# Optimization experiments

Hardware: AMD Instinct MI355X
Metric: run time of the kernel (lower is better)

Reference implementation:

```python
import jax, jax.numpy as jnp
import numpy as np

C = 1.0                      # Poincare ball curvature (pmath.project k=1.0)
SQRT_C = jnp.float32(np.sqrt(C))
MIN_NORM = 1e-15
BALL_EPS = 4e-3              # geoopt float32 boundary eps


def _norm(x):
    return jnp.clip(jnp.linalg.norm(x, axis=-1, keepdims=True), MIN_NORM, None)


def _artanh(x):
    return jnp.arctanh(jnp.clip(x, -1 + 1e-7, 1 - 1e-7))


def logmap0(x):
    # tangent vector at origin: artanh(sqrt(c)||x||) * x / (sqrt(c)||x||)
    n = _norm(x)
    return _artanh(SQRT_C * n) * x / (SQRT_C * n)


def expmap0(u):
    # point on ball: tanh(sqrt(c)||u||) * u / (sqrt(c)||u||)
    n = _norm(u)
    return jnp.tanh(SQRT_C * n) * u / (SQRT_C * n)


def project(x):
    # clip to open ball of radius (1-eps)/sqrt(c)
    n = _norm(x)
    maxnorm = (1.0 - BALL_EPS) / SQRT_C
    return jnp.where(n > maxnorm, x * (maxnorm / n), x)


def setup_inputs() -> dict:
    key = jax.random.key(0)
    k1, k2 = jax.random.split(key)
    B, N, D = 2, 8192, 256
    # valid Poincare-ball points: small tangent vectors mapped onto the ball
    x = project(expmap0(0.1 * jax.random.normal(k1, (B, N, D), dtype=jnp.float32)))
    # row-normalized-ish dense adjacency standing in for the sparse adj
    adj = jax.random.uniform(k2, (B, N, N), dtype=jnp.float32) / N
    return {"x": x, "adj": adj}


def reference(x, adj) -> jnp.ndarray:
    # HypAgg.forward: aggregate in tangent space at origin, map back, project
    x_tangent = logmap0(x)                          # [B, N, D]
    support_t = jnp.einsum("bij,bjd->bid", adj, x_tangent)  # batched spmm
    return project(expmap0(support_t))              # [B, N, D]
```

## Files before the change

kernel.cpp:

```cpp
#include <hip/hip_runtime.h>

#define BATCH 2
#define NN 8192
#define DD 256
#define BK 64

typedef __attribute__((ext_vector_type(8))) short bf16x8;
typedef __attribute__((ext_vector_type(4))) float f32x4;

__device__ __forceinline__ unsigned short f2bf(float f) {
    unsigned u = __builtin_bit_cast(unsigned, f);
    u += 0x7fffu + ((u >> 16) & 1u);
    return (unsigned short)(u >> 16);
}

__global__ void k_logmap_scale(const float* __restrict__ x, float* __restrict__ scale) {
    int row = blockIdx.x;
    int lane = threadIdx.x;
    const float4* xr = (const float4*)(x + (size_t)row * DD);
    float4 v = xr[lane];
    float s = v.x * v.x + v.y * v.y + v.z * v.z + v.w * v.w;
#pragma unroll
    for (int m = 1; m < 64; m <<= 1) s += __shfl_xor(s, m, 64);
    if (lane == 0) {
        float n = sqrtf(s);
        n = fmaxf(n, 1e-15f);
        float z = fminf(n, 1.0f - 1e-7f);
        float at = 0.5f * logf((1.0f + z) / (1.0f - z));
        scale[row] = at / n;
    }
}

__global__ void k_transpose(const float* __restrict__ x, const float* __restrict__ scale,
                            unsigned short* __restrict__ xtf) {
    __shared__ __align__(16) unsigned short T[DD][72];
    int bid = blockIdx.x;
    int b = bid >> 7, kb = bid & 127;
    int bn0 = b * NN + kb * 64;
    int t = threadIdx.x;
    int r = t >> 2, cc = t & 3;
    float sc = scale[bn0 + r];
    const float4* rp = (const float4*)(x + (size_t)(bn0 + r) * DD + cc * 64);
#pragma unroll
    for (int j4 = 0; j4 < 16; ++j4) {
        float4 v = rp[j4];
        int d = cc * 64 + j4 * 4;
        T[d + 0][r] = f2bf(v.x * sc);
        T[d + 1][r] = f2bf(v.y * sc);
        T[d + 2][r] = f2bf(v.z * sc);
        T[d + 3][r] = f2bf(v.w * sc);
    }
    __syncthreads();
    unsigned short* outp = xtf + (size_t)(b * 128 + kb) * DD * 64;
    int dd = t >> 3, ccc = t & 7;
#pragma unroll
    for (int p = 0; p < 8; ++p) {
        int d = dd + 32 * p;
        bf16x8 val = *(const bf16x8*)&T[d][ccc * 8];
        *(bf16x8*)(outp + (size_t)d * 64 + ccc * 8) = val;
    }
}

__global__ __launch_bounds__(256, 1) void k_gemm(const float* __restrict__ adj,
                                                 const unsigned short* __restrict__ xtf,
                                                 float* __restrict__ out) {
    __shared__ __align__(16) unsigned short A_lds[64][72];
    __shared__ float red[4][64];
    __shared__ float rowscale[64];

    int bid = blockIdx.x;
    int xcd = bid & 7;
    int b = xcd >> 2;
    int mtile = ((bid >> 3) << 2) | (xcd & 3);
    int m0 = mtile * 64;

    int t = threadIdx.x;
    int w = t >> 6, lane = t & 63, c = lane & 15, q = lane >> 4;

    int ar = t >> 4;
    int ac4 = t & 15;
    const float* abase = adj + (size_t)b * NN * NN + (size_t)(m0 + ar) * NN + ac4 * 4;

    const unsigned short* xbase = xtf + (size_t)b * 128 * DD * 64
                                + (size_t)(w * 64 + c) * 64 + q * 8;

    f32x4 acc[4][4];
#pragma unroll
    for (int i = 0; i < 4; ++i)
#pragma unroll
        for (int j = 0; j < 4; ++j)
#pragma unroll
            for (int rg = 0; rg < 4; ++rg) acc[i][j][rg] = 0.0f;

    float4 av[4];
    bf16x8 bcur[4][2], bnxt[4][2];

#pragma unroll
    for (int i = 0; i < 4; ++i)
        av[i] = *(const float4*)(abase + (size_t)(i * 16) * NN);
#pragma unroll
    for (int nt = 0; nt < 4; ++nt)
#pragma unroll
        for (int kk = 0; kk < 2; ++kk)
            bcur[nt][kk] = *(const bf16x8*)(xbase + nt * 16 * 64 + kk * 32);

    for (int kb = 0; kb < 128; ++kb) {
#pragma unroll
        for (int i = 0; i < 4; ++i) {
            ushort4 pk;
            pk.x = f2bf(av[i].x); pk.y = f2bf(av[i].y);
            pk.z = f2bf(av[i].z); pk.w = f2bf(av[i].w);
            *(ushort4*)&A_lds[ar + i * 16][ac4 * 4] = pk;
        }
        __syncthreads();

        if (kb + 1 < 128) {
            const float* ab = abase + (size_t)(kb + 1) * BK;
#pragma unroll
            for (int i = 0; i < 4; ++i)
                av[i] = *(const float4*)(ab + (size_t)(i * 16) * NN);
            const unsigned short* xb = xbase + (size_t)(kb + 1) * DD * 64;
#pragma unroll
            for (int nt = 0; nt < 4; ++nt)
#pragma unroll
                for (int kk = 0; kk < 2; ++kk)
                    bnxt[nt][kk] = *(const bf16x8*)(xb + nt * 16 * 64 + kk * 32);
        }

#pragma unroll
        for (int kk = 0; kk < 2; ++kk) {
            bf16x8 af[4];
#pragma unroll
            for (int mt = 0; mt < 4; ++mt)
                af[mt] = *(const bf16x8*)&A_lds[mt * 16 + c][kk * 32 + q * 8];
#pragma unroll
            for (int mt = 0; mt < 4; ++mt)
#pragma unroll
                for (int nt = 0; nt < 4; ++nt)
                    acc[mt][nt] = __builtin_amdgcn_mfma_f32_16x16x32_bf16(
                        af[mt], bcur[nt][kk], acc[mt][nt], 0, 0, 0);
        }
        __syncthreads();

        if (kb + 1 < 128) {
#pragma unroll
            for (int nt = 0; nt < 4; ++nt)
#pragma unroll
                for (int kk = 0; kk < 2; ++kk)
                    bcur[nt][kk] = bnxt[nt][kk];
        }
    }

    float s[4][4];
#pragma unroll
    for (int mt = 0; mt < 4; ++mt)
#pragma unroll
        for (int rg = 0; rg < 4; ++rg) {
            float v = acc[mt][0][rg] * acc[mt][0][rg] + acc[mt][1][rg] * acc[mt][1][rg]
                    + acc[mt][2][rg] * acc[mt][2][rg] + acc[mt][3][rg] * acc[mt][3][rg];
            v += __shfl_xor(v, 1, 64);
            v += __shfl_xor(v, 2, 64);
            v += __shfl_xor(v, 4, 64);
            v += __shfl_xor(v, 8, 64);
            s[mt][rg] = v;
        }
#pragma unroll
    for (int mt = 0; mt < 4; ++mt)
#pragma unroll
        for (int rg = 0; rg < 4; ++rg)
            if (c == mt * 4 + rg)
                red[w][mt * 16 + q * 4 + rg] = s[mt][rg];
    __syncthreads();
    if (t < 64) {
        float tot = red[0][t] + red[1][t] + red[2][t] + red[3][t];
        float n = sqrtf(tot);
        n = fmaxf(n, 1e-15f);
        float th = tanhf(n);
        rowscale[t] = fminf(th, 1.0f - 4e-3f) / n;
    }
    __syncthreads();

    float* obase = out + ((size_t)b * NN + m0) * DD + w * 64 + c;
#pragma unroll
    for (int mt = 0; mt < 4; ++mt)
#pragma unroll
        for (int rg = 0; rg < 4; ++rg) {
            float rs = rowscale[mt * 16 + q * 4 + rg];
            float* orow = obase + (size_t)(mt * 16 + q * 4 + rg) * DD;
#pragma unroll
            for (int nt = 0; nt < 4; ++nt)
                orow[nt * 16] = acc[mt][nt][rg] * rs;
        }
}

extern "C" void kernel_launch(void* const* d_in, const int* in_sizes, int n_in,
                              void* d_out, int out_size, void* d_ws, size_t ws_size,
                              hipStream_t stream) {
    const float* x   = (const float*)d_in[0];
    const float* adj = (const float*)d_in[1];
    float* out = (float*)d_out;

    unsigned short* xtf = (unsigned short*)d_ws;
    float* scale = (float*)((char*)d_ws + (size_t)BATCH * 128 * DD * 64 * 2);

    k_logmap_scale<<<BATCH * NN, 64, 0, stream>>>(x, scale);
    k_transpose<<<BATCH * 128, 256, 0, stream>>>(x, scale, xtf);
    k_gemm<<<256, 256, 0, stream>>>(adj, xtf, out);
}
```

Before: 800.2 us.

## Fuse logmap norm into transpose prep and halve GEMM M-tile with double buffering

Merges the per-row logmap norm computation into the transpose/convert kernel, so each thread-quad computes the row norm from registers and one launch is removed. The GEMM tile height drops from 64 to 32 rows, doubling the grid to 512 blocks with launch bounds of 2 per CU so that all CUs are occupied. A is double-buffered in LDS with a two-step prefetch and one barrier per k-step. The trade-off is that the bf16 X tiles are re-read by twice as many blocks, adding L2 traffic.

Result: slower. 817.1 us (+2.1%).

```diff
diff --git a/kernel.cpp b/kernel.cpp
--- a/kernel.cpp
+++ b/kernel.cpp
@@ -14,41 +14,35 @@
     return (unsigned short)(u >> 16);
 }
 
-__global__ void k_logmap_scale(const float* __restrict__ x, float* __restrict__ scale) {
-    int row = blockIdx.x;
-    int lane = threadIdx.x;
-    const float4* xr = (const float4*)(x + (size_t)row * DD);
-    float4 v = xr[lane];
-    float s = v.x * v.x + v.y * v.y + v.z * v.z + v.w * v.w;
-#pragma unroll
-    for (int m = 1; m < 64; m <<= 1) s += __shfl_xor(s, m, 64);
-    if (lane == 0) {
-        float n = sqrtf(s);
-        n = fmaxf(n, 1e-15f);
-        float z = fminf(n, 1.0f - 1e-7f);
-        float at = 0.5f * logf((1.0f + z) / (1.0f - z));
-        scale[row] = at / n;
-    }
-}
-
-__global__ void k_transpose(const float* __restrict__ x, const float* __restrict__ scale,
-                            unsigned short* __restrict__ xtf) {
+__global__ __launch_bounds__(256) void k_prep(const float* __restrict__ x,
+                                              unsigned short* __restrict__ xtf) {
     __shared__ __align__(16) unsigned short T[DD][72];
     int bid = blockIdx.x;
     int b = bid >> 7, kb = bid & 127;
     int bn0 = b * NN + kb * 64;
     int t = threadIdx.x;
     int r = t >> 2, cc = t & 3;
-    float sc = scale[bn0 + r];
     const float4* rp = (const float4*)(x + (size_t)(bn0 + r) * DD + cc * 64);
-#pragma unroll
-    for (int j4 = 0; j4 < 16; ++j4) {
-        float4 v = rp[j4];
-        int d = cc * 64 + j4 * 4;
-        T[d + 0][r] = f2bf(v.x * sc);
-        T[d + 1][r] = f2bf(v.y * sc);
-        T[d + 2][r] = f2bf(v.z * sc);
-        T[d + 3][r] = f2bf(v.w * sc);
+    float4 v[16];
+    float s = 0.0f;
+#pragma unroll
+    for (int j = 0; j < 16; ++j) {
+        v[j] = rp[j];
+        s += v[j].x * v[j].x + v[j].y * v[j].y + v[j].z * v[j].z + v[j].w * v[j].w;
+    }
+    s += __shfl_xor(s, 1, 64);
+    s += __shfl_xor(s, 2, 64);
+    float n = fmaxf(sqrtf(s), 1e-15f);
+    float z = fminf(n, 1.0f - 1e-7f);
+    float at = 0.5f * logf((1.0f + z) / (1.0f - z));
+    float sc = at / n;
+#pragma unroll
+    for (int j = 0; j < 16; ++j) {
+        int d = cc * 64 + j * 4;
+        T[d + 0][r] = f2bf(v[j].x * sc);
+        T[d + 1][r] = f2bf(v[j].y * sc);
+        T[d + 2][r] = f2bf(v[j].z * sc);
+        T[d + 3][r] = f2bf(v[j].w * sc);
     }
     __syncthreads();
     unsigned short* outp = xtf + (size_t)(b * 128 + kb) * DD * 64;
@@ -61,18 +55,18 @@
     }
 }
 
-__global__ __launch_bounds__(256, 1) void k_gemm(const float* __restrict__ adj,
+__global__ __launch_bounds__(256, 2) void k_gemm(const float* __restrict__ adj,
                                                  const unsigned short* __restrict__ xtf,
                                                  float* __restrict__ out) {
-    __shared__ __align__(16) unsigned short A_lds[64][72];
-    __shared__ float red[4][64];
-    __shared__ float rowscale[64];
+    __shared__ __align__(16) unsigned short A_lds[2][32][72];
+    __shared__ float red[4][32];
+    __shared__ float rowscale[32];
 
     int bid = blockIdx.x;
     int xcd = bid & 7;
     int b = xcd >> 2;
     int mtile = ((bid >> 3) << 2) | (xcd & 3);
-    int m0 = mtile * 64;
+    int m0 = mtile * 32;
 
     int t = threadIdx.x;
     int w = t >> 6, lane = t & 63, c = lane & 15, q = lane >> 4;
@@ -84,76 +78,76 @@
     const unsigned short* xbase = xtf + (size_t)b * 128 * DD * 64
                                 + (size_t)(w * 64 + c) * 64 + q * 8;
 
-    f32x4 acc[4][4];
-#pragma unroll
-    for (int i = 0; i < 4; ++i)
+    f32x4 acc[2][4];
+#pragma unroll
+    for (int i = 0; i < 2; ++i)
 #pragma unroll
         for (int j = 0; j < 4; ++j)
 #pragma unroll
             for (int rg = 0; rg < 4; ++rg) acc[i][j][rg] = 0.0f;
 
-    float4 av[4];
-    bf16x8 bcur[4][2], bnxt[4][2];
-
-#pragma unroll
-    for (int i = 0; i < 4; ++i)
-        av[i] = *(const float4*)(abase + (size_t)(i * 16) * NN);
-#pragma unroll
-    for (int nt = 0; nt < 4; ++nt)
-#pragma unroll
-        for (int kk = 0; kk < 2; ++kk)
-            bcur[nt][kk] = *(const bf16x8*)(xbase + nt * 16 * 64 + kk * 32);
-
-    for (int kb = 0; kb < 128; ++kb) {
-#pragma unroll
-        for (int i = 0; i < 4; ++i) {
-            ushort4 pk;
-            pk.x = f2bf(av[i].x); pk.y = f2bf(av[i].y);
-            pk.z = f2bf(av[i].z); pk.w = f2bf(av[i].w);
-            *(ushort4*)&A_lds[ar + i * 16][ac4 * 4] = pk;
+    float4 av[2][2];
+    bf16x8 bfr[2][4][2];
+
+#pragma unroll
+    for (int p = 0; p < 2; ++p) {
+        const float* ab = abase + (size_t)p * BK;
+#pragma unroll
+        for (int i = 0; i < 2; ++i)
+            av[p][i] = *(const float4*)(ab + (size_t)(i * 16) * NN);
+        const unsigned short* xb = xbase + (size_t)p * DD * 64;
+#pragma unroll
+        for (int nt = 0; nt < 4; ++nt)
+#pragma unroll
+            for (int kk = 0; kk < 2; ++kk)
+                bfr[p][nt][kk] = *(const bf16x8*)(xb + nt * 16 * 64 + kk * 32);
+    }
+
+    for (int kb2 = 0; kb2 < 128; kb2 += 2) {
+#pragma unroll
+        for (int p = 0; p < 2; ++p) {
+            int kb = kb2 + p;
+#pragma unroll
+            for (int i = 0; i < 2; ++i) {
+                ushort4 pk;
+                pk.x = f2bf(av[p][i].x); pk.y = f2bf(av[p][i].y);
+                pk.z = f2bf(av[p][i].z); pk.w = f2bf(av[p][i].w);
+                *(ushort4*)&A_lds[p][ar + i * 16][ac4 * 4] = pk;
+            }
+            if (kb + 2 < 128) {
+                const float* ab = abase + (size_t)(kb + 2) * BK;
+#pragma unroll
+                for (int i = 0; i < 2; ++i)
+                    av[p][i] = *(const float4*)(ab + (size_t)(i * 16) * NN);
+            }
+            __syncthreads();
+#pragma unroll
+            for (int kk = 0; kk < 2; ++kk) {
+                bf16x8 af[2];
+#pragma unroll
+                for (int mt = 0; mt < 2; ++mt)
+                    af[mt] = *(const bf16x8*)&A_lds[p][mt * 16 + c][kk * 32 + q * 8];
+#pragma unroll
+                for (int mt = 0; mt < 2; ++mt)
+#pragma unroll
+                    for (int nt = 0; nt < 4; ++nt)
+                        acc[mt][nt] = __builtin_amdgcn_mfma_f32_16x16x32_bf16(
+                            af[mt], bfr[p][nt][kk], acc[mt][nt], 0, 0, 0);
+            }
+            if (kb + 2 < 128) {
+                const unsigned short* xb = xbase + (size_t)(kb + 2) * DD * 64;
+#pragma unroll
+                for (int nt = 0; nt < 4; ++nt)
+#pragma unroll
+                    for (int kk = 0; kk < 2; ++kk)
+                        bfr[p][nt][kk] = *(const bf16x8*)(xb + nt * 16 * 64 + kk * 32);
+            }
         }
-        __syncthreads();
-
-        if (kb + 1 < 128) {
-            const float* ab = abase + (size_t)(kb + 1) * BK;
-#pragma unroll
-            for (int i = 0; i < 4; ++i)
-                av[i] = *(const float4*)(ab + (size_t)(i * 16) * NN);
-            const unsigned short* xb = xbase + (size_t)(kb + 1) * DD * 64;
-#pragma unroll
-            for (int nt = 0; nt < 4; ++nt)
-#pragma unroll
-                for (int kk = 0; kk < 2; ++kk)
-                    bnxt[nt][kk] = *(const bf16x8*)(xb + nt * 16 * 64 + kk * 32);
-        }
-
-#pragma unroll
-        for (int kk = 0; kk < 2; ++kk) {
-            bf16x8 af[4];
-#pragma unroll
-            for (int mt = 0; mt < 4; ++mt)
-                af[mt] = *(const bf16x8*)&A_lds[mt * 16 + c][kk * 32 + q * 8];
-#pragma unroll
-            for (int mt = 0; mt < 4; ++mt)
-#pragma unroll
-                for (int nt = 0; nt < 4; ++nt)
-                    acc[mt][nt] = __builtin_amdgcn_mfma_f32_16x16x32_bf16(
-                        af[mt], bcur[nt][kk], acc[mt][nt], 0, 0, 0);
-        }
-        __syncthreads();
-
-        if (kb + 1 < 128) {
-#pragma unroll
-            for (int nt = 0; nt < 4; ++nt)
-#pragma unroll
-                for (int kk = 0; kk < 2; ++kk)
-                    bcur[nt][kk] = bnxt[nt][kk];
-        }
-    }
-
-    float s[4][4];
-#pragma unroll
-    for (int mt = 0; mt < 4; ++mt)
+    }
+
+    float sred[2][4];
+#pragma unroll
+    for (int mt = 0; mt < 2; ++mt)
 #pragma unroll
         for (int rg = 0; rg < 4; ++rg) {
             float v = acc[mt][0][rg] * acc[mt][0][rg] + acc[mt][1][rg] * acc[mt][1][rg]
@@ -162,19 +156,18 @@
             v += __shfl_xor(v, 2, 64);
             v += __shfl_xor(v, 4, 64);
             v += __shfl_xor(v, 8, 64);
-            s[mt][rg] = v;
+            sred[mt][rg] = v;
         }
 #pragma unroll
-    for (int mt = 0; mt < 4; ++mt)
+    for (int mt = 0; mt < 2; ++mt)
 #pragma unroll
         for (int rg = 0; rg < 4; ++rg)
             if (c == mt * 4 + rg)
-                red[w][mt * 16 + q * 4 + rg] = s[mt][rg];
+                red[w][mt * 16 + q * 4 + rg] = sred[mt][rg];
     __syncthreads();
-    if (t < 64) {
+    if (t < 32) {
         float tot = red[0][t] + red[1][t] + red[2][t] + red[3][t];
-        float n = sqrtf(tot);
-        n = fmaxf(n, 1e-15f);
+        float n = fmaxf(sqrtf(tot), 1e-15f);
         float th = tanhf(n);
         rowscale[t] = fminf(th, 1.0f - 4e-3f) / n;
     }
@@ -182,7 +175,7 @@
 
     float* obase = out + ((size_t)b * NN + m0) * DD + w * 64 + c;
 #pragma unroll
-    for (int mt = 0; mt < 4; ++mt)
+    for (int mt = 0; mt < 2; ++mt)
 #pragma unroll
         for (int rg = 0; rg < 4; ++rg) {
             float rs = rowscale[mt * 16 + q * 4 + rg];
@@ -201,9 +194,7 @@
     float* out = (float*)d_out;
 
     unsigned short* xtf = (unsigned short*)d_ws;
-    float* scale = (float*)((char*)d_ws + (size_t)BATCH * 128 * DD * 64 * 2);
-
-    k_logmap_scale<<<BATCH * NN, 64, 0, stream>>>(x, scale);
-    k_transpose<<<BATCH * 128, 256, 0, stream>>>(x, scale, xtf);
-    k_gemm<<<256, 256, 0, stream>>>(adj, xtf, out);
-}
+
+    k_prep<<<BATCH * 128, 256, 0, stream>>>(x, xtf);
+    k_gemm<<<512, 256, 0, stream>>>(adj, xtf, out);
+}
```
